# Kernel tuning notes

Measured on AMD Instinct MI355X. Metric: run time of the kernel, lower is better.

## Reference

```python
import jax, jax.numpy as jnp
import numpy as np

# ---- static config (mirrors GridEncoder.__init__ kwargs) ----
INPUT_DIM = 3
NUM_LEVELS = 3          # CUDA wrapper hardcodes L = 3
LEVEL_DIM = 2           # C
PER_LEVEL_SCALE = 2.0
BASE_RESOLUTION = 128   # H
LOG2_HASHMAP_SIZE = 19
ALIGN_CORNERS = False
INTERP_ID = 0           # 0 = linear, 1 = smoothstep
B = 2097152             # number of query points
PLANE_H, PLANE_W = 1024, 512  # 3*PLANE_H*PLANE_W == offsets[-1]
PRIMES = (1, 2654435761, 805459861)  # instant-NGP spatial hash primes
S = float(np.log2(PER_LEVEL_SCALE))


def _compute_offsets():
    # replicates GridEncoder.__init__ offset construction
    offsets, offset = [], 0
    max_params = 2 ** LOG2_HASHMAP_SIZE
    for i in range(NUM_LEVELS):
        resolution = int(np.ceil(BASE_RESOLUTION * PER_LEVEL_SCALE ** i))
        params = min(max_params, (resolution if ALIGN_CORNERS else resolution + 1) ** INPUT_DIM)
        params = int(np.ceil(params / 8) * 8)
        offsets.append(offset)
        offset += params
    offsets.append(offset)
    return offsets


def setup_inputs() -> dict:
    key = jax.random.key(0)
    k1, k2 = jax.random.split(key)
    total = _compute_offsets()[-1]
    assert 3 * PLANE_H * PLANE_W == total, (total,)
    # learned triplane feature maps (embeddings.normal_(0, 0.1) in reset_parameters)
    triplane = 0.1 * jax.random.normal(k1, (3, LEVEL_DIM, PLANE_H, PLANE_W), dtype=jnp.float32)
    # query coordinates in [-bound, bound] = [-1, 1]
    inputs = jax.random.uniform(k2, (B, INPUT_DIM), dtype=jnp.float32, minval=-1.0, maxval=1.0)
    return {"triplane": triplane, "inputs": inputs}


def _grid_encode(x01, embeddings):
    # x01: [B, D] in [0,1]; embeddings: [offsets[-1], C] flat multi-level table
    offsets = _compute_offsets()
    D, C = INPUT_DIM, LEVEL_DIM
    n_corners = 2 ** D
    # binary corner offsets [8, 3]
    corners = jnp.array([[(i >> d) & 1 for d in range(D)] for i in range(n_corners)],
                        dtype=jnp.uint32)
    out = jnp.zeros((x01.shape[0], C), dtype=embeddings.dtype)
    for level in range(NUM_LEVELS):
        scale = 2.0 ** (level * S) * BASE_RESOLUTION - 1.0
        res = int(np.ceil(scale)) + 1
        hmap = offsets[level + 1] - offsets[level]
        pos = x01 * scale + (0.0 if ALIGN_CORNERS else 0.5)
        pos_grid = jnp.floor(pos)
        frac = pos - pos_grid                      # [B, D] in [0,1)
        if INTERP_ID == 1:  # smoothstep
            frac = frac * frac * (3.0 - 2.0 * frac)
        pg = pos_grid.astype(jnp.uint32)
        cp = pg[:, None, :] + corners[None, :, :]  # [B, 8, D] corner coords
        stride_dim = res if ALIGN_CORNERS else res + 1
        if stride_dim ** D > hmap:  # hash indexing (uint32 mult wraps, as in CUDA)
            p = jnp.array(PRIMES, dtype=jnp.uint32)
            h = cp * p
            idx = h[..., 0] ^ h[..., 1] ^ h[..., 2]
        else:  # dense (tiled) indexing
            strides = jnp.array([stride_dim ** d for d in range(D)], dtype=jnp.uint32)
            idx = jnp.sum(cp * strides, axis=-1, dtype=jnp.uint32)
        idx = (idx % jnp.uint32(hmap)).astype(jnp.int32) + offsets[level]  # [B, 8]
        feats = embeddings[idx]                    # [B, 8, C] gather
        # trilinear weights: prod over dims of frac / (1-frac) per corner bit
        w = jnp.prod(jnp.where(corners[None].astype(bool),
                               frac[:, None, :], 1.0 - frac[:, None, :]), axis=-1)  # [B, 8]
        out = out + jnp.einsum('bk,bkc->bc', w, feats)
    return out


def reference(triplane, inputs):
    bound = 1.0
    x01 = (inputs + bound) / (2.0 * bound)  # map to [0, 1]
    # triplane_.squeeze().permute(0,2,3,1).reshape(-1, level_dim)
    emb = jnp.transpose(triplane, (0, 2, 3, 1)).reshape(-1, LEVEL_DIM)
    return _grid_encode(x01, emb)  # [B, C]
```

## Files before the change

### kernel.cpp

```cpp
#include <hip/hip_runtime.h>
#include <hip/hip_fp16.h>


#define NPOINTS  2097152
#define HMASK    0x7FFFFu
#define PLANE    524288
#define NTAB     (3 * PLANE)
#define GBLOCKS  2048
#define TTHREADS (GBLOCKS * 256)
#define PPT      4

typedef float    floatx2 __attribute__((ext_vector_type(2)));
typedef unsigned uintx2  __attribute__((ext_vector_type(2)));
typedef unsigned uintx4  __attribute__((ext_vector_type(4)));

__device__ __forceinline__ unsigned pack2(float a, float b) {
    const __half2 h2 = __halves2half2(__float2half_rn(a), __float2half_rn(b));
    return *reinterpret_cast<const unsigned*>(&h2);
}

__global__ __launch_bounds__(256) void tp_convert_kernel(
    const float* __restrict__ tp, uintx4* __restrict__ tbl)
{
    const unsigned t = blockIdx.x * 256u + threadIdx.x;
    const unsigned level = t >> 17;
    const unsigned i4    = (t & 131071u) << 2;
    const float* __restrict__ b = tp + level * (2u * PLANE);
    const float4 c0 = *reinterpret_cast<const float4*>(b + i4);
    const float4 c1 = *reinterpret_cast<const float4*>(b + PLANE + i4);
    uintx4 o;
    o.x = pack2(c0.x, c1.x);
    o.y = pack2(c0.y, c1.y);
    o.z = pack2(c0.z, c1.z);
    o.w = pack2(c0.w, c1.w);
    tbl[t] = o;
}

__device__ __forceinline__ unsigned sel4(uintx4 q, unsigned o) {
    const unsigned a = (o & 1u) ? q.y : q.x;
    const unsigned b = (o & 1u) ? q.w : q.z;
    return (o & 2u) ? b : a;
}

__global__ __launch_bounds__(256) void grid_gather_kernel(
    const unsigned* __restrict__ tbl,
    const float* __restrict__ inputs,
    floatx2* __restrict__ out)
{
    const int t = blockIdx.x * 256 + threadIdx.x;

    float x0[PPT], y0[PPT], z0[PPT];
#pragma unroll
    for (int p = 0; p < PPT; ++p) {
        const int i = t + p * TTHREADS;
        const float x = __builtin_nontemporal_load(&inputs[3 * i + 0]);
        const float y = __builtin_nontemporal_load(&inputs[3 * i + 1]);
        const float z = __builtin_nontemporal_load(&inputs[3 * i + 2]);
        x0[p] = (x + 1.0f) * 0.5f;
        y0[p] = (y + 1.0f) * 0.5f;
        z0[p] = (z + 1.0f) * 0.5f;
    }

    float o0[PPT], o1[PPT];
#pragma unroll
    for (int p = 0; p < PPT; ++p) { o0[p] = 0.0f; o1[p] = 0.0f; }

#pragma unroll
    for (int level = 0; level < 3; ++level) {
        const float scale = (float)((128 << level) - 1);
        const unsigned lvl = (unsigned)level << 19;

#pragma unroll
        for (int p = 0; p < PPT; ++p) {
            const float px = fmaf(x0[p], scale, 0.5f);
            const float py = fmaf(y0[p], scale, 0.5f);
            const float pz = fmaf(z0[p], scale, 0.5f);
            const float fx = floorf(px), fy = floorf(py), fz = floorf(pz);
            const float rx = px - fx, ry = py - fy, rz = pz - fz;
            const unsigned gx = (unsigned)fx, gy = (unsigned)fy, gz = (unsigned)fz;

            const unsigned d = gx ^ (gx + 1u);
            const unsigned hy0 = gy * 2654435761u;
            const unsigned hy1 = (gy + 1u) * 2654435761u;
            const unsigned hz0 = gz * 805459861u;
            const unsigned hz1 = (gz + 1u) * 805459861u;

            unsigned P0[4];
            P0[0] = lvl | ((gx ^ hy0 ^ hz0) & HMASK);
            P0[1] = lvl | ((gx ^ hy1 ^ hz0) & HMASK);
            P0[2] = lvl | ((gx ^ hy0 ^ hz1) & HMASK);
            P0[3] = lvl | ((gx ^ hy1 ^ hz1) & HMASK);

            unsigned e0[4], e1[4];
            if (d == 1u) {
#pragma unroll
                for (int j = 0; j < 4; ++j) {
                    const unsigned P = P0[j];
                    const uintx2 q = *reinterpret_cast<const uintx2*>(tbl + (P & ~1u));
                    const unsigned o = P & 1u;
                    e0[j] = o ? q.y : q.x;
                    e1[j] = o ? q.x : q.y;
                }
            } else if (d == 3u) {
#pragma unroll
                for (int j = 0; j < 4; ++j) {
                    const unsigned P = P0[j];
                    const uintx4 q = *reinterpret_cast<const uintx4*>(tbl + (P & ~3u));
                    const unsigned o = P & 3u;
                    e0[j] = sel4(q, o);
                    e1[j] = sel4(q, o ^ 3u);
                }
            } else {
#pragma unroll
                for (int j = 0; j < 4; ++j) {
                    const unsigned P = P0[j];
                    e0[j] = tbl[P];
                    e1[j] = tbl[P ^ d];
                }
            }

            const float wx1 = rx, wx0 = 1.0f - rx;
            const float wy1 = ry, wy0 = 1.0f - ry;
            const float wz1 = rz, wz0 = 1.0f - rz;
            const float wyz[4] = { wy0 * wz0, wy1 * wz0, wy0 * wz1, wy1 * wz1 };
#pragma unroll
            for (int j = 0; j < 4; ++j) {
                const __half2 a = *reinterpret_cast<const __half2*>(&e0[j]);
                const __half2 b = *reinterpret_cast<const __half2*>(&e1[j]);
                const float2 fa = __half22float2(a);
                const float2 fb = __half22float2(b);
                const float wA = wx0 * wyz[j], wB = wx1 * wyz[j];
                o0[p] = fmaf(wA, fa.x, o0[p]); o1[p] = fmaf(wA, fa.y, o1[p]);
                o0[p] = fmaf(wB, fb.x, o0[p]); o1[p] = fmaf(wB, fb.y, o1[p]);
            }
        }
        __syncthreads();
    }

#pragma unroll
    for (int p = 0; p < PPT; ++p) {
        floatx2 r; r.x = o0[p]; r.y = o1[p];
        __builtin_nontemporal_store(r, &out[t + p * TTHREADS]);
    }
}

__global__ __launch_bounds__(256) void grid_fallback_kernel(
    const float* __restrict__ triplane,
    const float* __restrict__ inputs,
    float* __restrict__ out)
{
    const int i = blockIdx.x * blockDim.x + threadIdx.x;
    if (i >= NPOINTS) return;
    const float x0 = (inputs[3 * i + 0] + 1.0f) * 0.5f;
    const float y0 = (inputs[3 * i + 1] + 1.0f) * 0.5f;
    const float z0 = (inputs[3 * i + 2] + 1.0f) * 0.5f;
    float o0 = 0.0f, o1 = 0.0f;
#pragma unroll
    for (int level = 0; level < 3; ++level) {
        const float scale = (float)((128 << level) - 1);
        const float px = fmaf(x0, scale, 0.5f);
        const float py = fmaf(y0, scale, 0.5f);
        const float pz = fmaf(z0, scale, 0.5f);
        const float fx = floorf(px), fy = floorf(py), fz = floorf(pz);
        const float rx = px - fx, ry = py - fy, rz = pz - fz;
        const unsigned gx = (unsigned)fx, gy = (unsigned)fy, gz = (unsigned)fz;
        const float* __restrict__ base = triplane + level * (2 * PLANE);
#pragma unroll
        for (int c = 0; c < 8; ++c) {
            const unsigned bx = (c >> 0) & 1, by = (c >> 1) & 1, bz = (c >> 2) & 1;
            const unsigned h = (gx + bx) ^ ((gy + by) * 2654435761u) ^ ((gz + bz) * 805459861u);
            const unsigned local = h & HMASK;
            const float w = (bx ? rx : 1.0f - rx) * (by ? ry : 1.0f - ry) * (bz ? rz : 1.0f - rz);
            o0 = fmaf(w, base[local], o0);
            o1 = fmaf(w, base[PLANE + local], o1);
        }
    }
    reinterpret_cast<float2*>(out)[i] = make_float2(o0, o1);
}

extern "C" void kernel_launch(void* const* d_in, const int* in_sizes, int n_in,
                              void* d_out, int out_size, void* d_ws, size_t ws_size,
                              hipStream_t stream) {
    const float* triplane = (const float*)d_in[0];
    const float* inputs   = (const float*)d_in[1];
    const int threads = 256;

    if (ws_size >= (size_t)NTAB * sizeof(unsigned)) {
        unsigned* tbl = (unsigned*)d_ws;
        tp_convert_kernel<<<(NTAB / 4) / threads, threads, 0, stream>>>(
            triplane, (uintx4*)tbl);
        grid_gather_kernel<<<GBLOCKS, threads, 0, stream>>>(tbl, inputs, (floatx2*)d_out);
    } else {
        grid_fallback_kernel<<<NPOINTS / threads, threads, 0, stream>>>(
            triplane, inputs, (float*)d_out);
    }
}
```

Baseline: 198.4 us.

## Fuse table conversion and gather into one kernel with grid barrier

Merges the fp16 table-conversion kernel and the gather kernel into one persistent launch of 1024 blocks. The blocks synchronise through a global atomic counter used as a grid-wide barrier, and each thread then handles two sweeps of four points. This removes one kernel launch and the gap between kernels. In exchange it adds a memset, the barrier spin, and fewer blocks in flight, and it relies on all 1024 blocks being co-resident, otherwise the barrier can deadlock.

```diff
diff --git a/kernel.cpp b/kernel.cpp
--- a/kernel.cpp
+++ b/kernel.cpp
@@ -6,8 +6,10 @@
 #define HMASK    0x7FFFFu
 #define PLANE    524288
 #define NTAB     (3 * PLANE)
-#define GBLOCKS  2048
-#define TTHREADS (GBLOCKS * 256)
+#define NQUADS   (NTAB / 4)
+#define CBLOCKS  1024
+#define CTHREADS (CBLOCKS * 256)
+#define SWEEPS   2
 #define PPT      4
 
 typedef float    floatx2 __attribute__((ext_vector_type(2)));
@@ -19,12 +21,17 @@
     return *reinterpret_cast<const unsigned*>(&h2);
 }
 
-__global__ __launch_bounds__(256) void tp_convert_kernel(
-    const float* __restrict__ tp, uintx4* __restrict__ tbl)
+__device__ __forceinline__ unsigned sel4(uintx4 q, unsigned o) {
+    const unsigned a = (o & 1u) ? q.y : q.x;
+    const unsigned b = (o & 1u) ? q.w : q.z;
+    return (o & 2u) ? b : a;
+}
+
+__device__ __forceinline__ void convert_quad(
+    const float* __restrict__ tp, uintx4* __restrict__ tbl4, unsigned q)
 {
-    const unsigned t = blockIdx.x * 256u + threadIdx.x;
-    const unsigned level = t >> 17;
-    const unsigned i4    = (t & 131071u) << 2;
+    const unsigned level = q >> 17;
+    const unsigned i4    = (q & 131071u) << 2;
     const float* __restrict__ b = tp + level * (2u * PLANE);
     const float4 c0 = *reinterpret_cast<const float4*>(b + i4);
     const float4 c1 = *reinterpret_cast<const float4*>(b + PLANE + i4);
@@ -33,114 +40,129 @@
     o.y = pack2(c0.y, c1.y);
     o.z = pack2(c0.z, c1.z);
     o.w = pack2(c0.w, c1.w);
-    tbl[t] = o;
-}
-
-__device__ __forceinline__ unsigned sel4(uintx4 q, unsigned o) {
-    const unsigned a = (o & 1u) ? q.y : q.x;
-    const unsigned b = (o & 1u) ? q.w : q.z;
-    return (o & 2u) ? b : a;
-}
-
-__global__ __launch_bounds__(256) void grid_gather_kernel(
-    const unsigned* __restrict__ tbl,
+    tbl4[q] = o;
+}
+
+__global__ __launch_bounds__(256, 4) void grid_fused_kernel(
+    const float* __restrict__ triplane,
     const float* __restrict__ inputs,
+    unsigned* __restrict__ tbl,
+    unsigned* __restrict__ counter,
     floatx2* __restrict__ out)
 {
     const int t = blockIdx.x * 256 + threadIdx.x;
 
-    float x0[PPT], y0[PPT], z0[PPT];
-#pragma unroll
-    for (int p = 0; p < PPT; ++p) {
-        const int i = t + p * TTHREADS;
-        const float x = __builtin_nontemporal_load(&inputs[3 * i + 0]);
-        const float y = __builtin_nontemporal_load(&inputs[3 * i + 1]);
-        const float z = __builtin_nontemporal_load(&inputs[3 * i + 2]);
-        x0[p] = (x + 1.0f) * 0.5f;
-        y0[p] = (y + 1.0f) * 0.5f;
-        z0[p] = (z + 1.0f) * 0.5f;
-    }
-
-    float o0[PPT], o1[PPT];
-#pragma unroll
-    for (int p = 0; p < PPT; ++p) { o0[p] = 0.0f; o1[p] = 0.0f; }
-
-#pragma unroll
-    for (int level = 0; level < 3; ++level) {
-        const float scale = (float)((128 << level) - 1);
-        const unsigned lvl = (unsigned)level << 19;
-
+    {
+        uintx4* tbl4 = reinterpret_cast<uintx4*>(tbl);
+        convert_quad(triplane, tbl4, (unsigned)t);
+        const unsigned q2 = (unsigned)t + (unsigned)CTHREADS;
+        if (q2 < (unsigned)NQUADS) convert_quad(triplane, tbl4, q2);
+    }
+
+    __syncthreads();
+    if (threadIdx.x == 0) {
+        __threadfence();
+        atomicAdd(counter, 1u);
+        while (atomicAdd(counter, 0u) < (unsigned)CBLOCKS)
+            __builtin_amdgcn_s_sleep(2);
+        __threadfence();
+    }
+    __syncthreads();
+
+    for (int sweep = 0; sweep < SWEEPS; ++sweep) {
+        float x0[PPT], y0[PPT], z0[PPT];
 #pragma unroll
         for (int p = 0; p < PPT; ++p) {
-            const float px = fmaf(x0[p], scale, 0.5f);
-            const float py = fmaf(y0[p], scale, 0.5f);
-            const float pz = fmaf(z0[p], scale, 0.5f);
-            const float fx = floorf(px), fy = floorf(py), fz = floorf(pz);
-            const float rx = px - fx, ry = py - fy, rz = pz - fz;
-            const unsigned gx = (unsigned)fx, gy = (unsigned)fy, gz = (unsigned)fz;
-
-            const unsigned d = gx ^ (gx + 1u);
-            const unsigned hy0 = gy * 2654435761u;
-            const unsigned hy1 = (gy + 1u) * 2654435761u;
-            const unsigned hz0 = gz * 805459861u;
-            const unsigned hz1 = (gz + 1u) * 805459861u;
-
-            unsigned P0[4];
-            P0[0] = lvl | ((gx ^ hy0 ^ hz0) & HMASK);
-            P0[1] = lvl | ((gx ^ hy1 ^ hz0) & HMASK);
-            P0[2] = lvl | ((gx ^ hy0 ^ hz1) & HMASK);
-            P0[3] = lvl | ((gx ^ hy1 ^ hz1) & HMASK);
-
-            unsigned e0[4], e1[4];
-            if (d == 1u) {
+            const int i = t + (sweep * PPT + p) * CTHREADS;
+            const float x = __builtin_nontemporal_load(&inputs[3 * i + 0]);
+            const float y = __builtin_nontemporal_load(&inputs[3 * i + 1]);
+            const float z = __builtin_nontemporal_load(&inputs[3 * i + 2]);
+            x0[p] = (x + 1.0f) * 0.5f;
+            y0[p] = (y + 1.0f) * 0.5f;
+            z0[p] = (z + 1.0f) * 0.5f;
+        }
+
+        float o0[PPT], o1[PPT];
+#pragma unroll
+        for (int p = 0; p < PPT; ++p) { o0[p] = 0.0f; o1[p] = 0.0f; }
+
+#pragma unroll
+        for (int level = 0; level < 3; ++level) {
+            const float scale = (float)((128 << level) - 1);
+            const unsigned lvl = (unsigned)level << 19;
+
+#pragma unroll
+            for (int p = 0; p < PPT; ++p) {
+                const float px = fmaf(x0[p], scale, 0.5f);
+                const float py = fmaf(y0[p], scale, 0.5f);
+                const float pz = fmaf(z0[p], scale, 0.5f);
+                const float fx = floorf(px), fy = floorf(py), fz = floorf(pz);
+                const float rx = px - fx, ry = py - fy, rz = pz - fz;
+                const unsigned gx = (unsigned)fx, gy = (unsigned)fy, gz = (unsigned)fz;
+
+                const unsigned d = gx ^ (gx + 1u);
+                const unsigned hy0 = gy * 2654435761u;
+                const unsigned hy1 = (gy + 1u) * 2654435761u;
+                const unsigned hz0 = gz * 805459861u;
+                const unsigned hz1 = (gz + 1u) * 805459861u;
+
+                unsigned P0[4];
+                P0[0] = lvl | ((gx ^ hy0 ^ hz0) & HMASK);
+                P0[1] = lvl | ((gx ^ hy1 ^ hz0) & HMASK);
+                P0[2] = lvl | ((gx ^ hy0 ^ hz1) & HMASK);
+                P0[3] = lvl | ((gx ^ hy1 ^ hz1) & HMASK);
+
+                unsigned e0[4], e1[4];
+                if (d == 1u) {
+#pragma unroll
+                    for (int j = 0; j < 4; ++j) {
+                        const unsigned P = P0[j];
+                        const uintx2 q = *reinterpret_cast<const uintx2*>(tbl + (P & ~1u));
+                        const unsigned o = P & 1u;
+                        e0[j] = o ? q.y : q.x;
+                        e1[j] = o ? q.x : q.y;
+                    }
+                } else if (d == 3u) {
+#pragma unroll
+                    for (int j = 0; j < 4; ++j) {
+                        const unsigned P = P0[j];
+                        const uintx4 q = *reinterpret_cast<const uintx4*>(tbl + (P & ~3u));
+                        const unsigned o = P & 3u;
+                        e0[j] = sel4(q, o);
+                        e1[j] = sel4(q, o ^ 3u);
+                    }
+                } else {
+#pragma unroll
+                    for (int j = 0; j < 4; ++j) {
+                        const unsigned P = P0[j];
+                        e0[j] = tbl[P];
+                        e1[j] = tbl[P ^ d];
+                    }
+                }
+
+                const float wx1 = rx, wx0 = 1.0f - rx;
+                const float wy1 = ry, wy0 = 1.0f - ry;
+                const float wz1 = rz, wz0 = 1.0f - rz;
+                const float wyz[4] = { wy0 * wz0, wy1 * wz0, wy0 * wz1, wy1 * wz1 };
 #pragma unroll
                 for (int j = 0; j < 4; ++j) {
-                    const unsigned P = P0[j];
-                    const uintx2 q = *reinterpret_cast<const uintx2*>(tbl + (P & ~1u));
-                    const unsigned o = P & 1u;
-                    e0[j] = o ? q.y : q.x;
-                    e1[j] = o ? q.x : q.y;
-                }
-            } else if (d == 3u) {
-#pragma unroll
-                for (int j = 0; j < 4; ++j) {
-                    const unsigned P = P0[j];
-                    const uintx4 q = *reinterpret_cast<const uintx4*>(tbl + (P & ~3u));
-                    const unsigned o = P & 3u;
-                    e0[j] = sel4(q, o);
-                    e1[j] = sel4(q, o ^ 3u);
-                }
-            } else {
-#pragma unroll
-                for (int j = 0; j < 4; ++j) {
-                    const unsigned P = P0[j];
-                    e0[j] = tbl[P];
-                    e1[j] = tbl[P ^ d];
+                    const __half2 a = *reinterpret_cast<const __half2*>(&e0[j]);
+                    const __half2 b = *reinterpret_cast<const __half2*>(&e1[j]);
+                    const float2 fa = __half22float2(a);
+                    const float2 fb = __half22float2(b);
+                    const float wA = wx0 * wyz[j], wB = wx1 * wyz[j];
+                    o0[p] = fmaf(wA, fa.x, o0[p]); o1[p] = fmaf(wA, fa.y, o1[p]);
+                    o0[p] = fmaf(wB, fb.x, o0[p]); o1[p] = fmaf(wB, fb.y, o1[p]);
                 }
             }
-
-            const float wx1 = rx, wx0 = 1.0f - rx;
-            const float wy1 = ry, wy0 = 1.0f - ry;
-            const float wz1 = rz, wz0 = 1.0f - rz;
-            const float wyz[4] = { wy0 * wz0, wy1 * wz0, wy0 * wz1, wy1 * wz1 };
-#pragma unroll
-            for (int j = 0; j < 4; ++j) {
-                const __half2 a = *reinterpret_cast<const __half2*>(&e0[j]);
-                const __half2 b = *reinterpret_cast<const __half2*>(&e1[j]);
-                const float2 fa = __half22float2(a);
-                const float2 fb = __half22float2(b);
-                const float wA = wx0 * wyz[j], wB = wx1 * wyz[j];
-                o0[p] = fmaf(wA, fa.x, o0[p]); o1[p] = fmaf(wA, fa.y, o1[p]);
-                o0[p] = fmaf(wB, fb.x, o0[p]); o1[p] = fmaf(wB, fb.y, o1[p]);
-            }
-        }
-        __syncthreads();
-    }
-
-#pragma unroll
-    for (int p = 0; p < PPT; ++p) {
-        floatx2 r; r.x = o0[p]; r.y = o1[p];
-        __builtin_nontemporal_store(r, &out[t + p * TTHREADS]);
+            __syncthreads();
+        }
+
+#pragma unroll
+        for (int p = 0; p < PPT; ++p) {
+            floatx2 r; r.x = o0[p]; r.y = o1[p];
+            __builtin_nontemporal_store(r, &out[t + (sweep * PPT + p) * CTHREADS]);
+        }
     }
 }
 
@@ -183,15 +205,15 @@
                               hipStream_t stream) {
     const float* triplane = (const float*)d_in[0];
     const float* inputs   = (const float*)d_in[1];
-    const int threads = 256;
-
-    if (ws_size >= (size_t)NTAB * sizeof(unsigned)) {
+
+    if (ws_size >= (size_t)NTAB * sizeof(unsigned) + 64) {
         unsigned* tbl = (unsigned*)d_ws;
-        tp_convert_kernel<<<(NTAB / 4) / threads, threads, 0, stream>>>(
-            triplane, (uintx4*)tbl);
-        grid_gather_kernel<<<GBLOCKS, threads, 0, stream>>>(tbl, inputs, (floatx2*)d_out);
+        unsigned* counter = tbl + NTAB;
+        hipMemsetAsync(counter, 0, sizeof(unsigned), stream);
+        grid_fused_kernel<<<CBLOCKS, 256, 0, stream>>>(
+            triplane, inputs, tbl, counter, (floatx2*)d_out);
     } else {
-        grid_fallback_kernel<<<NPOINTS / threads, threads, 0, stream>>>(
+        grid_fallback_kernel<<<NPOINTS / 256, 256, 0, stream>>>(
             triplane, inputs, (float*)d_out);
     }
 }
```

New measurement: 329.8 us. 1.66x slower.
